# Kernel tuning notes

Measured on AMD Instinct MI355X. Metric: run time of the kernel, lower is better.

The kernel has to match this reference:

```python
import jax, jax.numpy as jnp
import numpy as np

F = 1024
H = 16
DH = F // H  # 64
MLP = 4096
EPS = 1e-5


def layernorm(x, g, b):
    mu = x.mean(-1, keepdims=True)
    var = ((x - mu) ** 2).mean(-1, keepdims=True)
    return (x - mu) * jax.lax.rsqrt(var + EPS) * g + b


def softmax_off_by_one(a):
    e = jnp.exp(a - a.max(-1, keepdims=True))
    return e / (1.0 + e.sum(-1, keepdims=True))


def setup_inputs() -> dict:
    key = jax.random.key(0)
    ks = jax.random.split(key, 12)
    s = 0.02
    return {
        "x": jax.random.normal(ks[0], (2, 2048, F), jnp.float32),
        "ln1_g": jnp.ones((F,), jnp.float32),
        "ln1_b": jnp.zeros((F,), jnp.float32),
        "Wq": jax.random.normal(ks[1], (F, F), jnp.float32) * s,
        "bq": jnp.zeros((F,), jnp.float32),
        "Wk": jax.random.normal(ks[2], (F, F), jnp.float32) * s,
        "bk": jnp.zeros((F,), jnp.float32),
        "Wv": jax.random.normal(ks[3], (F, F), jnp.float32) * s,
        "bv": jnp.zeros((F,), jnp.float32),
        "Wo": jax.random.normal(ks[4], (F, F), jnp.float32) * s,
        "bo": jnp.zeros((F,), jnp.float32),
        "slim": jnp.ones((H,), jnp.float32),
        "ln2_g": jnp.ones((F,), jnp.float32),
        "ln2_b": jnp.zeros((F,), jnp.float32),
        "W1": jax.random.normal(ks[5], (F, MLP), jnp.float32) * s,
        "b1": jnp.zeros((MLP,), jnp.float32),
        "W2": jax.random.normal(ks[6], (MLP, F), jnp.float32) * s,
        "b2": jnp.zeros((F,), jnp.float32),
    }


def reference(x, ln1_g, ln1_b, Wq, bq, Wk, bk, Wv, bv, Wo, bo, slim,
              ln2_g, ln2_b, W1, b1, W2, b2):
    b, n, f = x.shape
    h = layernorm(x, ln1_g, ln1_b)
    # project and split heads: [b, H, n, DH]
    q = (h @ Wq + bq).reshape(b, n, H, DH).transpose(0, 2, 1, 3)
    k = (h @ Wk + bk).reshape(b, n, H, DH).transpose(0, 2, 1, 3)
    v = (h @ Wv + bv).reshape(b, n, H, DH).transpose(0, 2, 1, 3)
    att = jnp.einsum('bhid,bhjd->bhij', q, k) / (DH ** 0.5)
    probs = softmax_off_by_one(att)  # off-by-one softmax
    probs = probs * slim[None, :, None, None]  # slimming after softmax
    attn = jnp.einsum('bhij,bhjd->bihd', probs, v).reshape(b, n, F)
    out = attn @ Wo + bo + x  # residual 1
    h2 = layernorm(out, ln2_g, ln2_b)
    m = jax.nn.gelu(h2 @ W1 + b1, approximate=False)
    m = jax.nn.gelu(m @ W2 + b2, approximate=False)
    return m + out  # residual 2
```

## Files before the change

kernel.cpp:

```cpp
#include <hip/hip_runtime.h>
#include <hip/hip_bf16.h>

typedef __hip_bfloat16 bf16;
typedef short bf16x8 __attribute__((ext_vector_type(8)));
typedef short bf16x4 __attribute__((ext_vector_type(4)));
typedef float f32x4 __attribute__((ext_vector_type(4)));

__device__ __forceinline__ float gelu_f(float x) {
  return 0.5f * x * (1.f + erff(x * 0.70710678118654752f));
}

__device__ __forceinline__ unsigned short f2bfu(float f) {
  bf16 h = __float2bfloat16(f);
  unsigned short u;
  __builtin_memcpy(&u, &h, 2);
  return u;
}

__device__ __forceinline__ void load16_lds(const bf16* g, bf16* l) {
  __builtin_amdgcn_global_load_lds(
      (const __attribute__((address_space(1))) unsigned int*)g,
      (__attribute__((address_space(3))) unsigned int*)l, 16, 0, 0);
}

__global__ __launch_bounds__(256) void transpose_cast(
    const float* __restrict__ src, bf16* __restrict__ dst, int R, int C) {
  __shared__ float tile[32][33];
  int tx = threadIdx.x & 31, ty = threadIdx.x >> 5;
  int r0 = blockIdx.y * 32, c0 = blockIdx.x * 32;
  #pragma unroll
  for (int i = ty; i < 32; i += 8)
    tile[i][tx] = src[(size_t)(r0 + i) * C + (c0 + tx)];
  __syncthreads();
  #pragma unroll
  for (int i = ty; i < 32; i += 8)
    dst[(size_t)(c0 + i) * R + (r0 + tx)] = __float2bfloat16(tile[tx][i]);
}

__global__ __launch_bounds__(256) void ln_kernel(
    const float* __restrict__ x, const float* __restrict__ g,
    const float* __restrict__ b, bf16* __restrict__ y) {
  int row = blockIdx.x;
  int t = threadIdx.x;
  const float4* xr = (const float4*)(x + (size_t)row * 1024);
  float4 v = xr[t];
  float s = v.x + v.y + v.z + v.w;
  float ss = v.x * v.x + v.y * v.y + v.z * v.z + v.w * v.w;
  #pragma unroll
  for (int off = 32; off >= 1; off >>= 1) {
    s += __shfl_xor(s, off);
    ss += __shfl_xor(ss, off);
  }
  __shared__ float red[8];
  int wv = t >> 6;
  if ((t & 63) == 0) { red[wv] = s; red[4 + wv] = ss; }
  __syncthreads();
  float S = red[0] + red[1] + red[2] + red[3];
  float SS = red[4] + red[5] + red[6] + red[7];
  float mu = S * (1.f / 1024.f);
  float var = SS * (1.f / 1024.f) - mu * mu;
  float inv = rsqrtf(var + 1e-5f);
  float4 gv = ((const float4*)g)[t];
  float4 bv = ((const float4*)b)[t];
  ushort4 o;
  o.x = f2bfu((v.x - mu) * inv * gv.x + bv.x);
  o.y = f2bfu((v.y - mu) * inv * gv.y + bv.y);
  o.z = f2bfu((v.z - mu) * inv * gv.z + bv.z);
  o.w = f2bfu((v.w - mu) * inv * gv.w + bv.w);
  ((ushort4*)(y + (size_t)row * 1024))[t] = o;
}

template <int EPI>
__global__ __launch_bounds__(256) void gemm_bf16(
    const bf16* __restrict__ A, const bf16* __restrict__ Bt,
    const float* __restrict__ bias0, const float* __restrict__ resid,
    void* __restrict__ C0, int M, int N, int K) {
  __shared__ __align__(16) bf16 As[2][128 * 32];
  __shared__ __align__(16) bf16 Bs[2][128 * 32];
  const int t = threadIdx.x, lane = t & 63, w = t >> 6;
  const int wm = (w >> 1) * 64, wn = (w & 1) * 64;
  const int m0 = blockIdx.y * 128, n0 = blockIdx.x * 128;

  const int srow = lane >> 2;
  const int sgrp = lane & 3;
  f32x4 acc[4][4] = {};

  const bf16* Abase = A + (size_t)m0 * K;
  const bf16* Bbase = Bt + (size_t)n0 * K;

  auto stage = [&](int buf, int kt) {
    #pragma unroll
    for (int c = 0; c < 2; ++c) {
      int row = w * 32 + c * 16 + srow;
      int sw = (row & 3) ^ ((row >> 2) & 3);
      int gg = sgrp ^ sw;
      const bf16* ga = Abase + (size_t)row * K + kt + gg * 8;
      const bf16* gb = Bbase + (size_t)row * K + kt + gg * 8;
      load16_lds(ga, &As[buf][(w * 32 + c * 16) * 32]);
      load16_lds(gb, &Bs[buf][(w * 32 + c * 16) * 32]);
    }
  };

  const int q8 = (((lane >> 4) ^ (lane & 3) ^ ((lane >> 2) & 3))) * 8;
  const int fr = lane & 15;

  const int nk = K >> 5;
  stage(0, 0);
  for (int i = 0; i < nk; ++i) {
    const int cur = i & 1;
    __syncthreads();
    if (i + 1 < nk) stage(cur ^ 1, (i + 1) << 5);
    bf16x8 af[4], bfr[4];
    #pragma unroll
    for (int mc = 0; mc < 4; ++mc)
      af[mc] = *(const bf16x8*)&As[cur][(wm + mc * 16 + fr) * 32 + q8];
    #pragma unroll
    for (int nc = 0; nc < 4; ++nc)
      bfr[nc] = *(const bf16x8*)&Bs[cur][(wn + nc * 16 + fr) * 32 + q8];
    #pragma unroll
    for (int mc = 0; mc < 4; ++mc)
      #pragma unroll
      for (int nc = 0; nc < 4; ++nc)
        acc[mc][nc] = __builtin_amdgcn_mfma_f32_16x16x32_bf16(
            af[mc], bfr[nc], acc[mc][nc], 0, 0, 0);
  }

  #pragma unroll
  for (int mc = 0; mc < 4; ++mc) {
    #pragma unroll
    for (int reg = 0; reg < 4; ++reg) {
      int m = m0 + wm + mc * 16 + ((lane >> 4) << 2) + reg;
      #pragma unroll
      for (int nc = 0; nc < 4; ++nc) {
        int n = n0 + wn + nc * 16 + (lane & 15);
        float val = acc[mc][nc][reg] + bias0[n];
        size_t idx = (size_t)m * N + n;
        if constexpr (EPI == 3) {
          ((float*)C0)[idx] = val + resid[idx];
        }
      }
    }
  }
}

template <int EPI>
__global__ __launch_bounds__(512, 2) void gemm256(
    const bf16* __restrict__ A, const bf16* __restrict__ Bt,
    const float* __restrict__ bias0, const float* __restrict__ bias1,
    const float* __restrict__ bias2,
    void* __restrict__ C0, void* __restrict__ C1, void* __restrict__ C2,
    int M, int N, int K) {
  __shared__ __align__(16) bf16 As[2][256 * 64];
  __shared__ __align__(16) bf16 Bs[2][256 * 64];
  const int t = threadIdx.x, lane = t & 63, w = t >> 6;
  const int wm = (w >> 2) * 128, wn = (w & 3) * 64;
  const int m0 = blockIdx.y * 256, n0 = blockIdx.x * 256;
  const int koff = (EPI == 6) ? (int)blockIdx.z * 1024 : 0;
  const int nk = ((EPI == 6) ? 1024 : K) >> 6;

  const bf16* Abase = A + (size_t)m0 * K + koff;
  const bf16* Bbase = Bt + (size_t)n0 * K + koff;

  const int lrow = lane >> 3;
  const int lgrp = (lane & 7) ^ lrow;
  const size_t lgoff = (size_t)lrow * K + lgrp * 8;

  auto stageA = [&](int buf, int half, int tile) {
    const int r = half * 128 + w * 16;
    const bf16* g = Abase + (size_t)r * K + tile * 64 + lgoff;
    bf16* l = &As[buf][r * 64];
    load16_lds(g, l);
    load16_lds(g + (size_t)8 * K, l + 8 * 64);
  };
  auto stageB = [&](int buf, int half, int tile) {
    const int r = half * 128 + w * 16;
    const bf16* g = Bbase + (size_t)r * K + tile * 64 + lgoff;
    bf16* l = &Bs[buf][r * 64];
    load16_lds(g, l);
    load16_lds(g + (size_t)8 * K, l + 8 * 64);
  };

  const int fr = lane & 15, qd = lane >> 4, frs = fr & 7;
  const int ao0 = (qd ^ frs) * 8;
  const int ao1 = ((4 + qd) ^ frs) * 8;
  const int rowA = (wm + fr) * 64;
  const int rowB = (wn + fr) * 64;

  f32x4 acc[8][4] = {};

  stageA(0, 0, 0); stageA(0, 1, 0); stageB(0, 0, 0); stageB(0, 1, 0);
  stageA(1, 0, 1); stageA(1, 1, 1);
  asm volatile("s_waitcnt vmcnt(4)" ::: "memory");
  asm volatile("s_barrier" ::: "memory");

  for (int i = 0; i < nk; ++i) {
    const int c = i & 1;
    const bf16* as = &As[c][0];
    const bf16* bs = &Bs[c][0];
    bf16x8 aF[8][2], bF[4][2];

    #pragma unroll
    for (int mi = 0; mi < 4; ++mi) {
      aF[mi][0] = *(const bf16x8*)(as + rowA + mi * 1024 + ao0);
      aF[mi][1] = *(const bf16x8*)(as + rowA + mi * 1024 + ao1);
    }
    #pragma unroll
    for (int ni = 0; ni < 2; ++ni) {
      bF[ni][0] = *(const bf16x8*)(bs + rowB + ni * 1024 + ao0);
      bF[ni][1] = *(const bf16x8*)(bs + rowB + ni * 1024 + ao1);
    }
    if (i + 1 < nk) stageB(c ^ 1, 0, i + 1);
    asm volatile("s_barrier" ::: "memory");
    asm volatile("s_waitcnt lgkmcnt(0)" ::: "memory");
    __builtin_amdgcn_sched_barrier(0);
    __builtin_amdgcn_s_setprio(1);
    #pragma unroll
    for (int mi = 0; mi < 4; ++mi)
      #pragma unroll
      for (int ni = 0; ni < 2; ++ni) {
        acc[mi][ni] = __builtin_amdgcn_mfma_f32_16x16x32_bf16(
            aF[mi][0], bF[ni][0], acc[mi][ni], 0, 0, 0);
        acc[mi][ni] = __builtin_amdgcn_mfma_f32_16x16x32_bf16(
            aF[mi][1], bF[ni][1], acc[mi][ni], 0, 0, 0);
      }
    __builtin_amdgcn_s_setprio(0);
    __builtin_amdgcn_sched_barrier(0);
    asm volatile("s_barrier" ::: "memory");

    #pragma unroll
    for (int mi = 4; mi < 8; ++mi) {
      aF[mi][0] = *(const bf16x8*)(as + rowA + mi * 1024 + ao0);
      aF[mi][1] = *(const bf16x8*)(as + rowA + mi * 1024 + ao1);
    }
    #pragma unroll
    for (int ni = 2; ni < 4; ++ni) {
      bF[ni][0] = *(const bf16x8*)(bs + rowB + ni * 1024 + ao0);
      bF[ni][1] = *(const bf16x8*)(bs + rowB + ni * 1024 + ao1);
    }
    if (i + 1 < nk) stageB(c ^ 1, 1, i + 1);
    asm volatile("s_barrier" ::: "memory");
    asm volatile("s_waitcnt lgkmcnt(0)" ::: "memory");
    __builtin_amdgcn_sched_barrier(0);
    __builtin_amdgcn_s_setprio(1);
    #pragma unroll
    for (int mi = 4; mi < 8; ++mi)
      #pragma unroll
      for (int ni = 2; ni < 4; ++ni) {
        acc[mi][ni] = __builtin_amdgcn_mfma_f32_16x16x32_bf16(
            aF[mi][0], bF[ni][0], acc[mi][ni], 0, 0, 0);
        acc[mi][ni] = __builtin_amdgcn_mfma_f32_16x16x32_bf16(
            aF[mi][1], bF[ni][1], acc[mi][ni], 0, 0, 0);
      }
    __builtin_amdgcn_s_setprio(0);
    __builtin_amdgcn_sched_barrier(0);
    asm volatile("s_barrier" ::: "memory");

    if (i + 2 < nk) stageA(c, 0, i + 2);
    asm volatile("s_barrier" ::: "memory");
    __builtin_amdgcn_sched_barrier(0);
    __builtin_amdgcn_s_setprio(1);
    #pragma unroll
    for (int mi = 0; mi < 4; ++mi)
      #pragma unroll
      for (int ni = 2; ni < 4; ++ni) {
        acc[mi][ni] = __builtin_amdgcn_mfma_f32_16x16x32_bf16(
            aF[mi][0], bF[ni][0], acc[mi][ni], 0, 0, 0);
        acc[mi][ni] = __builtin_amdgcn_mfma_f32_16x16x32_bf16(
            aF[mi][1], bF[ni][1], acc[mi][ni], 0, 0, 0);
      }
    __builtin_amdgcn_s_setprio(0);
    __builtin_amdgcn_sched_barrier(0);
    asm volatile("s_barrier" ::: "memory");

    if (i + 2 < nk) {
      stageA(c, 1, i + 2);
      asm volatile("s_waitcnt vmcnt(4)" ::: "memory");
    } else {
      asm volatile("s_waitcnt vmcnt(0)" ::: "memory");
    }
    asm volatile("s_barrier" ::: "memory");
    __builtin_amdgcn_sched_barrier(0);
    __builtin_amdgcn_s_setprio(1);
    #pragma unroll
    for (int mi = 4; mi < 8; ++mi)
      #pragma unroll
      for (int ni = 0; ni < 2; ++ni) {
        acc[mi][ni] = __builtin_amdgcn_mfma_f32_16x16x32_bf16(
            aF[mi][0], bF[ni][0], acc[mi][ni], 0, 0, 0);
        acc[mi][ni] = __builtin_amdgcn_mfma_f32_16x16x32_bf16(
            aF[mi][1], bF[ni][1], acc[mi][ni], 0, 0, 0);
      }
    __builtin_amdgcn_s_setprio(0);
    __builtin_amdgcn_sched_barrier(0);
    asm volatile("s_barrier" ::: "memory");
  }

  if constexpr (EPI == 0) {
    const int which = n0 >> 10;
    const float* bp = which == 0 ? bias0 : which == 1 ? bias1 : bias2;
    bf16* qk = (bf16*)(which == 0 ? C0 : C1);
    const float qscale = 0.18033688011112042f;
    #pragma unroll
    for (int mi = 0; mi < 8; ++mi) {
      #pragma unroll
      for (int reg = 0; reg < 4; ++reg) {
        int m = m0 + wm + mi * 16 + qd * 4 + reg;
        int b = m >> 11, tok = m & 2047;
        #pragma unroll
        for (int ni = 0; ni < 4; ++ni) {
          int n = n0 + wn + ni * 16 + fr;
          int nn = n & 1023, hh = nn >> 6, d = n & 63;
          float val = acc[mi][ni][reg] + bp[nn];
          if (which == 2)
            ((bf16*)C2)[(size_t)((b * 16 + hh) * 64 + d) * 2048 + tok] =
                __float2bfloat16(val);
          else if (which == 0)
            qk[(size_t)((b * 16 + hh) * 2048 + tok) * 64 + d] =
                __float2bfloat16(val * qscale);
          else
            qk[(size_t)((b * 16 + hh) * 2048 + tok) * 64 + d] =
                __float2bfloat16(val);
        }
      }
    }
  } else if constexpr (EPI == 4) {
    #pragma unroll
    for (int mi = 0; mi < 8; ++mi) {
      #pragma unroll
      for (int reg = 0; reg < 4; ++reg) {
        int m = m0 + wm + mi * 16 + qd * 4 + reg;
        #pragma unroll
        for (int ni = 0; ni < 4; ++ni) {
          int n = n0 + wn + ni * 16 + fr;
          float val = acc[mi][ni][reg] + bias0[n];
          ((bf16*)C0)[(size_t)m * N + n] = __float2bfloat16(gelu_f(val));
        }
      }
    }
  } else {
    bf16* pout = (bf16*)C0 + (size_t)blockIdx.z * M * N;
    #pragma unroll
    for (int mi = 0; mi < 8; ++mi) {
      #pragma unroll
      for (int reg = 0; reg < 4; ++reg) {
        int m = m0 + wm + mi * 16 + qd * 4 + reg;
        #pragma unroll
        for (int ni = 0; ni < 4; ++ni) {
          int n = n0 + wn + ni * 16 + fr;
          pout[(size_t)m * N + n] = __float2bfloat16(acc[mi][ni][reg]);
        }
      }
    }
  }
}

__global__ __launch_bounds__(256) void reduce_mlp2(
    const bf16* __restrict__ part, const float* __restrict__ b2,
    const float* __restrict__ out1, float* __restrict__ out) {
  const int row = blockIdx.x, t = threadIdx.x;
  const size_t base = (size_t)row * 1024 + t * 4;
  float sum[4] = {0.f, 0.f, 0.f, 0.f};
  #pragma unroll
  for (int kc = 0; kc < 4; ++kc) {
    ushort4 u = *(const ushort4*)(part + (size_t)kc * 4096 * 1024 + base);
    unsigned short us[4] = {u.x, u.y, u.z, u.w};
    #pragma unroll
    for (int j = 0; j < 4; ++j) {
      bf16 h;
      __builtin_memcpy(&h, &us[j], 2);
      sum[j] += __bfloat162float(h);
    }
  }
  float4 bv = ((const float4*)b2)[t];
  float4 rv = *(const float4*)(out1 + base);
  float4 o;
  o.x = gelu_f(sum[0] + bv.x) + rv.x;
  o.y = gelu_f(sum[1] + bv.y) + rv.y;
  o.z = gelu_f(sum[2] + bv.z) + rv.z;
  o.w = gelu_f(sum[3] + bv.w) + rv.w;
  *(float4*)(out + base) = o;
}

__global__ __launch_bounds__(256) void attn_kernel(
    const bf16* __restrict__ q, const bf16* __restrict__ k,
    const bf16* __restrict__ vt, const float* __restrict__ slim,
    bf16* __restrict__ attn) {
  __shared__ __align__(16) bf16 Ks[64][72];
  __shared__ __align__(16) bf16 Vs[64][72];
  __shared__ __align__(16) bf16 Ps[4][2][16][72];

  const int t = threadIdx.x, lane = t & 63, w = t >> 6;
  const int fr = lane & 15, qd = lane >> 4;
  const int bh = blockIdx.y;
  const int q0 = blockIdx.x * 128;
  const size_t bhbase = (size_t)bh * 2048 * 64;

  bf16x8 qf[2][2];
  #pragma unroll
  for (int s = 0; s < 2; ++s) {
    const int qrow = q0 + s * 64 + w * 16 + fr;
    const bf16* qp = q + bhbase + (size_t)qrow * 64 + qd * 8;
    qf[s][0] = *(const bf16x8*)qp;
    qf[s][1] = *(const bf16x8*)(qp + 32);
  }

  const int r0 = t >> 3, g0 = t & 7;
  const bf16* kbase = k + bhbase + (size_t)r0 * 64 + g0 * 8;
  const bf16* vbase = vt + bhbase + (size_t)r0 * 2048 + g0 * 8;

  bf16x8 kreg0, kreg1, vreg0, vreg1;
  auto gload = [&](int j0) {
    kreg0 = *(const bf16x8*)(kbase + (size_t)j0 * 64);
    kreg1 = *(const bf16x8*)(kbase + (size_t)(j0 + 32) * 64);
    vreg0 = *(const bf16x8*)(vbase + j0);
    vreg1 = *(const bf16x8*)(vbase + (size_t)32 * 2048 + j0);
  };
  gload(0);

  f32x4 o_acc[2][4] = {};
  float m4[2][4] = {};
  float l4[2][4] = {};

  for (int it = 0; it < 32; ++it) {
    *(bf16x8*)&Ks[r0][g0 * 8] = kreg0;
    *(bf16x8*)&Ks[r0 + 32][g0 * 8] = kreg1;
    *(bf16x8*)&Vs[r0][g0 * 8] = vreg0;
    *(bf16x8*)&Vs[r0 + 32][g0 * 8] = vreg1;
    __syncthreads();
    if (it + 1 < 32) gload((it + 1) * 64);

    bf16x8 kf[4][2];
    #pragma unroll
    for (int nc = 0; nc < 4; ++nc) {
      int kr = nc * 16 + fr;
      kf[nc][0] = *(const bf16x8*)&Ks[kr][qd * 8];
      kf[nc][1] = *(const bf16x8*)&Ks[kr][32 + qd * 8];
    }

    f32x4 z[2][4];
    #pragma unroll
    for (int s = 0; s < 2; ++s)
      #pragma unroll
      for (int nc = 0; nc < 4; ++nc) {
        f32x4 zz = {};
        zz = __builtin_amdgcn_mfma_f32_16x16x32_bf16(kf[nc][0], qf[s][0], zz, 0, 0, 0);
        zz = __builtin_amdgcn_mfma_f32_16x16x32_bf16(kf[nc][1], qf[s][1], zz, 0, 0, 0);
        z[s][nc] = zz;
      }

    bf16x8 vf[4][2];
    #pragma unroll
    for (int dc = 0; dc < 4; ++dc) {
      int vr = dc * 16 + fr;
      vf[dc][0] = *(const bf16x8*)&Vs[vr][qd * 8];
      vf[dc][1] = *(const bf16x8*)&Vs[vr][32 + qd * 8];
    }

    #pragma unroll
    for (int s = 0; s < 2; ++s) {
      #pragma unroll
      for (int nc = 0; nc < 4; ++nc) {
        float p0 = __builtin_amdgcn_exp2f(z[s][nc][0]);
        float p1 = __builtin_amdgcn_exp2f(z[s][nc][1]);
        float p2 = __builtin_amdgcn_exp2f(z[s][nc][2]);
        float p3 = __builtin_amdgcn_exp2f(z[s][nc][3]);
        l4[s][nc] += (p0 + p1) + (p2 + p3);
        m4[s][nc] = fmaxf(m4[s][nc], fmaxf(fmaxf(p0, p1), fmaxf(p2, p3)));
        bf16x4 pk;
        pk[0] = (short)f2bfu(p0);
        pk[1] = (short)f2bfu(p1);
        pk[2] = (short)f2bfu(p2);
        pk[3] = (short)f2bfu(p3);
        *(bf16x4*)&Ps[w][s][fr][nc * 16 + qd * 4] = pk;
      }

      bf16x8 pf0 = *(const bf16x8*)&Ps[w][s][fr][qd * 8];
      bf16x8 pf1 = *(const bf16x8*)&Ps[w][s][fr][32 + qd * 8];
      #pragma unroll
      for (int dc = 0; dc < 4; ++dc) {
        o_acc[s][dc] = __builtin_amdgcn_mfma_f32_16x16x32_bf16(pf0, vf[dc][0], o_acc[s][dc], 0, 0, 0);
        o_acc[s][dc] = __builtin_amdgcn_mfma_f32_16x16x32_bf16(pf1, vf[dc][1], o_acc[s][dc], 0, 0, 0);
      }
    }
    __syncthreads();
  }

  const int b = bh >> 4, hh = bh & 15;
  const float sl = slim[hh];
  #pragma unroll
  for (int s = 0; s < 2; ++s) {
    float l_all = (l4[s][0] + l4[s][1]) + (l4[s][2] + l4[s][3]);
    float m_all = fmaxf(fmaxf(m4[s][0], m4[s][1]), fmaxf(m4[s][2], m4[s][3]));
    l_all += __shfl_xor(l_all, 16);
    m_all = fmaxf(m_all, __shfl_xor(m_all, 16));
    l_all += __shfl_xor(l_all, 32);
    m_all = fmaxf(m_all, __shfl_xor(m_all, 32));

    #pragma unroll
    for (int r = 0; r < 4; ++r) {
      float lr = __shfl(l_all, qd * 4 + r);
      float mr = __shfl(m_all, qd * 4 + r);
      float inv = sl / (mr + lr);
      int mrow = b * 2048 + q0 + s * 64 + w * 16 + qd * 4 + r;
      #pragma unroll
      for (int dc = 0; dc < 4; ++dc) {
        int col = hh * 64 + dc * 16 + fr;
        attn[(size_t)mrow * 1024 + col] = __float2bfloat16(o_acc[s][dc][r] * inv);
      }
    }
  }
}

extern "C" void kernel_launch(void* const* d_in, const int* in_sizes, int n_in,
                              void* d_out, int out_size, void* d_ws, size_t ws_size,
                              hipStream_t stream) {
  const float* x    = (const float*)d_in[0];
  const float* ln1g = (const float*)d_in[1];
  const float* ln1b = (const float*)d_in[2];
  const float* Wq   = (const float*)d_in[3];
  const float* bq   = (const float*)d_in[4];
  const float* Wk   = (const float*)d_in[5];
  const float* bk   = (const float*)d_in[6];
  const float* Wv   = (const float*)d_in[7];
  const float* bv   = (const float*)d_in[8];
  const float* Wo   = (const float*)d_in[9];
  const float* bo   = (const float*)d_in[10];
  const float* slim = (const float*)d_in[11];
  const float* ln2g = (const float*)d_in[12];
  const float* ln2b = (const float*)d_in[13];
  const float* W1   = (const float*)d_in[14];
  const float* b1   = (const float*)d_in[15];
  const float* W2   = (const float*)d_in[16];
  const float* b2   = (const float*)d_in[17];

  char* p = (char*)d_ws;
  auto take = [&](size_t nbytes) {
    char* r = p;
    p += (nbytes + 255) & ~(size_t)255;
    return r;
  };
  bf16* Wqkv_t = (bf16*)take((size_t)3072 * 1024 * 2);
  bf16* Wo_t = (bf16*)take((size_t)1024 * 1024 * 2);
  bf16* W1_t = (bf16*)take((size_t)4096 * 1024 * 2);
  bf16* W2_t = (bf16*)take((size_t)1024 * 4096 * 2);
  bf16* h1   = (bf16*)take((size_t)4096 * 1024 * 2);
  bf16* qb   = (bf16*)take((size_t)4096 * 1024 * 2);
  bf16* kb   = (bf16*)take((size_t)4096 * 1024 * 2);
  bf16* vtb  = (bf16*)take((size_t)4096 * 1024 * 2);
  bf16* attn = (bf16*)take((size_t)4096 * 1024 * 2);
  float* out1 = (float*)take((size_t)4096 * 1024 * 4);
  bf16* h2   = (bf16*)take((size_t)4096 * 1024 * 2);
  bf16* m1   = (bf16*)take((size_t)4096 * 4096 * 2);

  bf16* parts = h1;

  dim3 blk(256);
  dim3 blk512(512);

  transpose_cast<<<dim3(32, 32), blk, 0, stream>>>(Wq, Wqkv_t, 1024, 1024);
  transpose_cast<<<dim3(32, 32), blk, 0, stream>>>(Wk, Wqkv_t + (size_t)1024 * 1024, 1024, 1024);
  transpose_cast<<<dim3(32, 32), blk, 0, stream>>>(Wv, Wqkv_t + (size_t)2048 * 1024, 1024, 1024);
  transpose_cast<<<dim3(32, 32), blk, 0, stream>>>(Wo, Wo_t, 1024, 1024);
  transpose_cast<<<dim3(128, 32), blk, 0, stream>>>(W1, W1_t, 1024, 4096);
  transpose_cast<<<dim3(32, 128), blk, 0, stream>>>(W2, W2_t, 4096, 1024);

  ln_kernel<<<4096, blk, 0, stream>>>(x, ln1g, ln1b, h1);

  gemm256<0><<<dim3(12, 16), blk512, 0, stream>>>(
      h1, Wqkv_t, bq, bk, bv, qb, kb, vtb, 4096, 3072, 1024);

  attn_kernel<<<dim3(16, 32), blk, 0, stream>>>(qb, kb, vtb, slim, attn);

  gemm_bf16<3><<<dim3(8, 32), blk, 0, stream>>>(
      attn, Wo_t, bo, x, out1, 4096, 1024, 1024);

  ln_kernel<<<4096, blk, 0, stream>>>(out1, ln2g, ln2b, h2);

  gemm256<4><<<dim3(16, 16), blk512, 0, stream>>>(
      h2, W1_t, b1, nullptr, nullptr, m1, nullptr, nullptr, 4096, 4096, 1024);

  gemm256<6><<<dim3(4, 16, 4), blk512, 0, stream>>>(
      m1, W2_t, nullptr, nullptr, nullptr, parts, nullptr, nullptr,
      4096, 1024, 4096);
  reduce_mlp2<<<4096, blk, 0, stream>>>(parts, b2, out1, (float*)d_out);
}
```

Measured before the change: 483.6 us.

## Rotate GEMM main-loop phases so last MFMA quadrant overlaps next tile loads

Restructures the software-pipelined GEMM main loop so the final MFMA quadrant of each iteration is deferred into the next iteration, running after the next tile's A fragments are loaded. The A-half staging for tile i+1 moves into the loop, and the vmcnt wait counts are adjusted to match. Fragment registers are hoisted out of the loop so they persist across iterations, and a trailing quadrant runs after the loop. The aim is to hide LDS-read and barrier latency behind MFMA work. The cost is more complex wait-count bookkeeping and possible register-pressure changes.

Result: faster. 406.3 us (-16.0%).

```diff
diff --git a/kernel.cpp b/kernel.cpp
--- a/kernel.cpp
+++ b/kernel.cpp
@@ -187,23 +187,50 @@
   const int rowB = (wn + fr) * 64;
 
   f32x4 acc[8][4] = {};
+  bf16x8 aF[8][2], bF[4][2];
+
+#define MFMA_Q(MLO, NLO)                                                   \
+  _Pragma("unroll")                                                        \
+  for (int mi = (MLO); mi < (MLO) + 4; ++mi)                               \
+    _Pragma("unroll")                                                      \
+    for (int ni = (NLO); ni < (NLO) + 2; ++ni) {                           \
+      acc[mi][ni] = __builtin_amdgcn_mfma_f32_16x16x32_bf16(               \
+          aF[mi][0], bF[ni][0], acc[mi][ni], 0, 0, 0);                     \
+      acc[mi][ni] = __builtin_amdgcn_mfma_f32_16x16x32_bf16(               \
+          aF[mi][1], bF[ni][1], acc[mi][ni], 0, 0, 0);                     \
+    }
 
   stageA(0, 0, 0); stageA(0, 1, 0); stageB(0, 0, 0); stageB(0, 1, 0);
-  stageA(1, 0, 1); stageA(1, 1, 1);
-  asm volatile("s_waitcnt vmcnt(4)" ::: "memory");
+  stageA(1, 0, 1);
+  asm volatile("s_waitcnt vmcnt(6)" ::: "memory");
   asm volatile("s_barrier" ::: "memory");
 
   for (int i = 0; i < nk; ++i) {
     const int c = i & 1;
     const bf16* as = &As[c][0];
     const bf16* bs = &Bs[c][0];
-    bf16x8 aF[8][2], bF[4][2];
 
     #pragma unroll
     for (int mi = 0; mi < 4; ++mi) {
       aF[mi][0] = *(const bf16x8*)(as + rowA + mi * 1024 + ao0);
       aF[mi][1] = *(const bf16x8*)(as + rowA + mi * 1024 + ao1);
     }
+    if (i + 1 < nk) {
+      stageA(c ^ 1, 1, i + 1);
+      asm volatile("s_waitcnt vmcnt(4)" ::: "memory");
+    } else {
+      asm volatile("s_waitcnt vmcnt(0)" ::: "memory");
+    }
+    asm volatile("s_barrier" ::: "memory");
+    __builtin_amdgcn_sched_barrier(0);
+    if (i) {
+      __builtin_amdgcn_s_setprio(1);
+      MFMA_Q(4, 2)
+      __builtin_amdgcn_s_setprio(0);
+    }
+    __builtin_amdgcn_sched_barrier(0);
+    asm volatile("s_barrier" ::: "memory");
+
     #pragma unroll
     for (int ni = 0; ni < 2; ++ni) {
       bF[ni][0] = *(const bf16x8*)(bs + rowB + ni * 1024 + ao0);
@@ -214,15 +241,7 @@
     asm volatile("s_waitcnt lgkmcnt(0)" ::: "memory");
     __builtin_amdgcn_sched_barrier(0);
     __builtin_amdgcn_s_setprio(1);
-    #pragma unroll
-    for (int mi = 0; mi < 4; ++mi)
-      #pragma unroll
-      for (int ni = 0; ni < 2; ++ni) {
-        acc[mi][ni] = __builtin_amdgcn_mfma_f32_16x16x32_bf16(
-            aF[mi][0], bF[ni][0], acc[mi][ni], 0, 0, 0);
-        acc[mi][ni] = __builtin_amdgcn_mfma_f32_16x16x32_bf16(
-            aF[mi][1], bF[ni][1], acc[mi][ni], 0, 0, 0);
-      }
+    MFMA_Q(0, 0)
     __builtin_amdgcn_s_setprio(0);
     __builtin_amdgcn_sched_barrier(0);
     asm volatile("s_barrier" ::: "memory");
@@ -232,68 +251,40 @@
       aF[mi][0] = *(const bf16x8*)(as + rowA + mi * 1024 + ao0);
       aF[mi][1] = *(const bf16x8*)(as + rowA + mi * 1024 + ao1);
     }
+    if (i + 1 < nk) stageB(c ^ 1, 1, i + 1);
+    asm volatile("s_barrier" ::: "memory");
+    asm volatile("s_waitcnt lgkmcnt(0)" ::: "memory");
+    __builtin_amdgcn_sched_barrier(0);
+    __builtin_amdgcn_s_setprio(1);
+    MFMA_Q(4, 0)
+    __builtin_amdgcn_s_setprio(0);
+    __builtin_amdgcn_sched_barrier(0);
+    asm volatile("s_barrier" ::: "memory");
+
     #pragma unroll
     for (int ni = 2; ni < 4; ++ni) {
       bF[ni][0] = *(const bf16x8*)(bs + rowB + ni * 1024 + ao0);
       bF[ni][1] = *(const bf16x8*)(bs + rowB + ni * 1024 + ao1);
     }
-    if (i + 1 < nk) stageB(c ^ 1, 1, i + 1);
+    if (i + 2 < nk) stageA(c, 0, i + 2);
+    if (i + 1 < nk) {
+      if (i + 2 < nk) {
+        asm volatile("s_waitcnt vmcnt(6)" ::: "memory");
+      } else {
+        asm volatile("s_waitcnt vmcnt(4)" ::: "memory");
+      }
+    }
     asm volatile("s_barrier" ::: "memory");
     asm volatile("s_waitcnt lgkmcnt(0)" ::: "memory");
     __builtin_amdgcn_sched_barrier(0);
     __builtin_amdgcn_s_setprio(1);
-    #pragma unroll
-    for (int mi = 4; mi < 8; ++mi)
-      #pragma unroll
-      for (int ni = 2; ni < 4; ++ni) {
-        acc[mi][ni] = __builtin_amdgcn_mfma_f32_16x16x32_bf16(
-            aF[mi][0], bF[ni][0], acc[mi][ni], 0, 0, 0);
-        acc[mi][ni] = __builtin_amdgcn_mfma_f32_16x16x32_bf16(
-            aF[mi][1], bF[ni][1], acc[mi][ni], 0, 0, 0);
-      }
+    MFMA_Q(0, 2)
     __builtin_amdgcn_s_setprio(0);
     __builtin_amdgcn_sched_barrier(0);
     asm volatile("s_barrier" ::: "memory");
-
-    if (i + 2 < nk) stageA(c, 0, i + 2);
-    asm volatile("s_barrier" ::: "memory");
-    __builtin_amdgcn_sched_barrier(0);
-    __builtin_amdgcn_s_setprio(1);
-    #pragma unroll
-    for (int mi = 0; mi < 4; ++mi)
-      #pragma unroll
-      for (int ni = 2; ni < 4; ++ni) {
-        acc[mi][ni] = __builtin_amdgcn_mfma_f32_16x16x32_bf16(
-            aF[mi][0], bF[ni][0], acc[mi][ni], 0, 0, 0);
-        acc[mi][ni] = __builtin_amdgcn_mfma_f32_16x16x32_bf16(
-            aF[mi][1], bF[ni][1], acc[mi][ni], 0, 0, 0);
-      }
-    __builtin_amdgcn_s_setprio(0);
-    __builtin_amdgcn_sched_barrier(0);
-    asm volatile("s_barrier" ::: "memory");
-
-    if (i + 2 < nk) {
-      stageA(c, 1, i + 2);
-      asm volatile("s_waitcnt vmcnt(4)" ::: "memory");
-    } else {
-      asm volatile("s_waitcnt vmcnt(0)" ::: "memory");
-    }
-    asm volatile("s_barrier" ::: "memory");
-    __builtin_amdgcn_sched_barrier(0);
-    __builtin_amdgcn_s_setprio(1);
-    #pragma unroll
-    for (int mi = 4; mi < 8; ++mi)
-      #pragma unroll
-      for (int ni = 0; ni < 2; ++ni) {
-        acc[mi][ni] = __builtin_amdgcn_mfma_f32_16x16x32_bf16(
-            aF[mi][0], bF[ni][0], acc[mi][ni], 0, 0, 0);
-        acc[mi][ni] = __builtin_amdgcn_mfma_f32_16x16x32_bf16(
-            aF[mi][1], bF[ni][1], acc[mi][ni], 0, 0, 0);
-      }
-    __builtin_amdgcn_s_setprio(0);
-    __builtin_amdgcn_sched_barrier(0);
-    asm volatile("s_barrier" ::: "memory");
-  }
+  }
+  MFMA_Q(4, 2)
+#undef MFMA_Q
 
   if constexpr (EPI == 0) {
     const int which = n0 >> 10;
```
